# Optimization experiments

Hardware: AMD Instinct MI355X
Metric: run time of the kernel (lower is better)

The kernel has to match this reference:

```python
import jax, jax.numpy as jnp
import numpy as np

B, S, D, K = 32, 1024, 256, 1024
DECAY = 0.99
EPS = 1e-05          # EMA laplace epsilon
LN_EPS = 1e-05       # LayerNorm epsilon
COMMITMENT_COST = 0.25


def setup_inputs() -> dict:
    key = jax.random.key(0)
    k1, k2, k3 = jax.random.split(key, 3)
    inputs = jax.random.normal(k1, (B, S, D), jnp.float32)
    # nn.Embedding init: uniform(-1/K, 1/K)
    weight = jax.random.uniform(k2, (K, D), jnp.float32, -1.0 / K, 1.0 / K)
    ema_w = jax.random.normal(k3, (K, D), jnp.float32)
    ema_cluster_size = jnp.zeros((K,), jnp.float32)
    ln_gamma = jnp.ones((D,), jnp.float32)
    ln_beta = jnp.zeros((D,), jnp.float32)
    return {"inputs": inputs, "weight": weight, "ema_w": ema_w,
            "ema_cluster_size": ema_cluster_size,
            "ln_gamma": ln_gamma, "ln_beta": ln_beta}


def _layernorm(x, g, b):
    mu = jnp.mean(x, axis=-1, keepdims=True)
    var = jnp.mean((x - mu) ** 2, axis=-1, keepdims=True)
    return (x - mu) * jax.lax.rsqrt(var + LN_EPS) * g + b


def reference(inputs, weight, ema_w, ema_cluster_size, ln_gamma, ln_beta):
    flat_input = inputs.reshape(-1, D)          # [N, D] (unnormalized, used for EMA dw)
    feats = _layernorm(flat_input, ln_gamma, ln_beta)  # norm_input in sample()

    # euclidean distances ||f||^2 + ||w||^2 - 2 f w^T  -> [N, K]
    d = (jnp.sum(feats ** 2, axis=1, keepdims=True)
         + jnp.sum(weight ** 2, axis=1)
         - 2.0 * feats @ weight.T)

    sampled_dist = jnp.min(d, axis=1)           # [N]
    idx_flat = jnp.argmin(d, axis=1)            # [N] int

    # faithful reproduction of the source's reordering:
    # argsort per batch row (values in [0,S)) then flat-index into the [N]-long index vector
    order = jnp.argsort(sampled_dist.reshape(B, S), axis=1).reshape(-1)  # [N], values in [0,S)
    enc_idx = idx_flat[order]                   # [N]

    quantized = weight[enc_idx].reshape(B, S, D)

    # ---- EMA codebook update (training path), no gradients ----
    fi = jax.lax.stop_gradient(flat_input)
    counts = jax.ops.segment_sum(jnp.ones((B * S,), jnp.float32), enc_idx,
                                 num_segments=K)                    # encodings.sum(0)
    new_cs = ema_cluster_size * DECAY + (1.0 - DECAY) * counts
    n = jnp.sum(new_cs)
    new_cs = (new_cs + EPS) / (n + K * EPS) * n
    dw = jax.ops.segment_sum(fi, enc_idx, num_segments=K)            # encodings.T @ flat_input
    new_ema_w = jax.lax.stop_gradient(ema_w) * DECAY + (1.0 - DECAY) * dw
    new_weight = new_ema_w / new_cs[:, None]

    # ---- losses (avg=False, loss_type=0) ----
    e_latent = jnp.mean((jax.lax.stop_gradient(quantized) - inputs) ** 2)
    q_latent = jnp.mean((quantized - jax.lax.stop_gradient(inputs)) ** 2)
    loss = q_latent + COMMITMENT_COST * e_latent

    # straight-through estimator
    quantized_st = inputs + jax.lax.stop_gradient(quantized - inputs)

    avg_probs = counts / (B * S)
    perplexity = jnp.exp(-jnp.sum(avg_probs * jnp.log(avg_probs + 1e-10)))

    return quantized_st, loss, perplexity, enc_idx, new_weight, new_ema_w, new_cs
```

## Files before the change

kernel.cpp:

```cpp
#include <hip/hip_runtime.h>
#include <cmath>

#define B_ 32
#define S_ 1024
#define D_ 256
#define K_ 1024
#define N_ (B_*S_)

#define O_Q     0
#define O_LOSS  8388608
#define O_PERP  8388609
#define O_IDX   8388610
#define O_NW    8421378
#define O_NEW   8683522
#define O_NCS   8945666

#define OFF_FH    0ull
#define OFF_WH    16777216ull
#define OFF_BW    17301504ull
#define OFF_BWF   17309696ull
#define OFF_SAMP  17313792ull
#define OFF_IDXF  17575936ull
#define OFF_ENC   17707008ull
#define OFF_CNT   17838080ull
#define OFF_SLOWC 17842176ull
#define OFF_SLOWL 17842240ull
#define OFF_LOSSP 17973312ull
#define OFF_COFF  18235456ull
#define OFF_CUR   18239552ull
#define OFF_ROWL  18243648ull

#define MARGIN 4e-5f

typedef _Float16 f16x8 __attribute__((ext_vector_type(8)));
typedef _Float16 f16x4 __attribute__((ext_vector_type(4)));
typedef float    f32x4 __attribute__((ext_vector_type(4)));

#define GL16(gp, lp) __builtin_amdgcn_global_load_lds( \
    (const __attribute__((address_space(1))) unsigned int*)(const void*)(gp), \
    (__attribute__((address_space(3))) unsigned int*)(void*)(lp), 16, 0, 0)

__global__ void k_pre(const float* __restrict__ x, const float* __restrict__ gam,
                      const float* __restrict__ bet, _Float16* __restrict__ fh,
                      const float* __restrict__ w, double* __restrict__ Bw,
                      float* __restrict__ Bwf, _Float16* __restrict__ wh) {
    int lane = threadIdx.x & 63, wv = threadIdx.x >> 6;
    if (blockIdx.x < N_ / 4) {
        int n = blockIdx.x * 4 + wv;
        const float4 xv = ((const float4*)(x + (size_t)n * D_))[lane];
        const float4 gv = ((const float4*)gam)[lane];
        const float4 bv = ((const float4*)bet)[lane];
        float s = xv.x + xv.y + xv.z + xv.w;
        for (int m = 32; m > 0; m >>= 1) s += __shfl_xor(s, m, 64);
        float mu = s * (1.0f / 256.0f);
        float c0 = xv.x - mu, c1 = xv.y - mu, c2 = xv.z - mu, c3 = xv.w - mu;
        float vs = c0 * c0 + c1 * c1 + c2 * c2 + c3 * c3;
        for (int m = 32; m > 0; m >>= 1) vs += __shfl_xor(vs, m, 64);
        float inv = 1.0f / sqrtf(vs * (1.0f / 256.0f) + 1e-5f);
        f16x4 o;
        o[0] = (_Float16)(c0 * inv * gv.x + bv.x);
        o[1] = (_Float16)(c1 * inv * gv.y + bv.y);
        o[2] = (_Float16)(c2 * inv * gv.z + bv.z);
        o[3] = (_Float16)(c3 * inv * gv.w + bv.w);
        *(f16x4*)&fh[(size_t)n * D_ + lane * 4] = o;
    } else {
        int k = (blockIdx.x - N_ / 4) * 4 + wv;
        const float4 v = ((const float4*)(w + (size_t)k * D_))[lane];
        double s = (double)v.x * v.x + (double)v.y * v.y
                 + (double)v.z * v.z + (double)v.w * v.w;
        for (int m = 32; m > 0; m >>= 1) s += __shfl_xor(s, m, 64);
        f16x4 o;
        o[0] = (_Float16)v.x; o[1] = (_Float16)v.y;
        o[2] = (_Float16)v.z; o[3] = (_Float16)v.w;
        *(f16x4*)&wh[(size_t)k * D_ + lane * 4] = o;
        if (lane == 0) { Bw[k] = s; Bwf[k] = (float)s; }
    }
}

__launch_bounds__(512, 4)
__global__ void k_phase1(const _Float16* __restrict__ fh, const _Float16* __restrict__ wh,
                         const float* __restrict__ Bwf, float* __restrict__ pq) {
    __shared__ __align__(16) _Float16 sA[3][128][32];
    __shared__ __align__(16) _Float16 sB[3][256][32];

    const int tid = threadIdx.x;
    const int lane = tid & 63;
    const int w = tid >> 6;
    const int wr = w >> 2;
    const int wc = w & 3;
    const int l15 = lane & 15;
    const int g = lane >> 4;
    const int id = blockIdx.x;
    const int grp = (id & 7) * 32 + (id >> 5);
    const int chunk = (id >> 3) & 3;
    const int row0 = grp * 128;
    const int c0 = chunk * 256;

    const int srow = lane >> 2;
    const int scol = (lane & 3) * 8;
    const _Float16* gp[3];
    int lrow[3]; int isA[3];
#pragma unroll
    for (int j = 0; j < 3; j++) {
        int li = w * 3 + j;
        if (li < 8) {
            isA[j] = 1; lrow[j] = li * 16;
            gp[j] = fh + (size_t)(row0 + li * 16 + srow) * 256 + scol;
        } else {
            isA[j] = 0; lrow[j] = (li - 8) * 16;
            gp[j] = wh + (size_t)(c0 + (li - 8) * 16 + srow) * 256 + scol;
        }
    }

    f32x4 acc[4][4];
#pragma unroll
    for (int a = 0; a < 4; a++)
#pragma unroll
        for (int b = 0; b < 4; b++) acc[a][b] = (f32x4){0.f, 0.f, 0.f, 0.f};

#define STAGE(bi, kk) do { \
    const int eoff_ = (kk) * 32; \
    _Pragma("unroll") \
    for (int j_ = 0; j_ < 3; j_++) { \
        if (isA[j_]) GL16(gp[j_] + eoff_, &sA[bi][lrow[j_]][0]); \
        else         GL16(gp[j_] + eoff_, &sB[bi][lrow[j_]][0]); \
    } \
} while (0)

    STAGE(0, 0);
    STAGE(1, 1);
    asm volatile("s_waitcnt vmcnt(3)" ::: "memory");
    __builtin_amdgcn_s_barrier();
    __builtin_amdgcn_sched_barrier(0);

#pragma unroll
    for (int ks = 0; ks < 8; ks++) {
        const int cur = ks % 3;
        if (ks < 6) STAGE((ks + 2) % 3, ks + 2);

        f16x8 cfr[4];
#pragma unroll
        for (int cb = 0; cb < 4; cb++)
            cfr[cb] = *(const f16x8*)&sB[cur][wc * 64 + cb * 16 + l15][g * 8];
        __builtin_amdgcn_s_setprio(1);
#pragma unroll
        for (int rb = 0; rb < 4; rb++) {
            f16x8 rf = *(const f16x8*)&sA[cur][wr * 64 + rb * 16 + l15][g * 8];
#pragma unroll
            for (int cb = 0; cb < 4; cb++)
                acc[cb][rb] = __builtin_amdgcn_mfma_f32_16x16x32_f16(
                    cfr[cb], rf, acc[cb][rb], 0, 0, 0);
        }
        __builtin_amdgcn_s_setprio(0);
        __builtin_amdgcn_sched_barrier(0);

        if (ks < 6)       asm volatile("s_waitcnt vmcnt(3)" ::: "memory");
        else if (ks == 6) asm volatile("s_waitcnt vmcnt(0)" ::: "memory");
        if (ks < 7) {
            __builtin_amdgcn_s_barrier();
            __builtin_amdgcn_sched_barrier(0);
        }
    }
#undef STAGE
    __syncthreads();

    float bwv[4][4];
#pragma unroll
    for (int cb = 0; cb < 4; cb++)
#pragma unroll
        for (int r = 0; r < 4; r++)
            bwv[cb][r] = Bwf[c0 + wc * 64 + cb * 16 + g * 4 + r];

    float* red = (float*)&sA[0][0][0];
#pragma unroll
    for (int rb = 0; rb < 4; rb++) {
        float m1 = 3e38f, m2 = 3e38f; int c1 = 0x7fffffff;
#pragma unroll
        for (int cb = 0; cb < 4; cb++) {
#pragma unroll
            for (int r = 0; r < 4; r++) {
                float sv = fmaf(-2.0f, acc[cb][rb][r], bwv[cb][r]);
                int c = c0 + wc * 64 + cb * 16 + g * 4 + r;
                if (sv < m1 || (sv == m1 && c < c1)) { m2 = m1; m1 = sv; c1 = c; }
                else if (sv < m2) m2 = sv;
            }
        }
#pragma unroll
        for (int msk = 16; msk <= 32; msk <<= 1) {
            float om1 = __shfl_xor(m1, msk, 64);
            float om2 = __shfl_xor(m2, msk, 64);
            int   oc  = __shfl_xor(c1, msk, 64);
            if (om1 < m1 || (om1 == m1 && oc < c1)) {
                m2 = (m1 < om2) ? m1 : om2; m1 = om1; c1 = oc;
            } else {
                m2 = (om1 < m2) ? om1 : m2;
            }
        }
        if (lane < 16) {
            int rl = wr * 64 + rb * 16 + l15;
            int base = (rl * 4 + wc) * 3;
            red[base] = m1; red[base + 1] = m2; ((int*)red)[base + 2] = c1;
        }
    }
    __syncthreads();
    if (tid < 128) {
        float M1 = 3e38f, M2 = 3e38f; int C1 = 0x7fffffff;
        for (int q = 0; q < 4; q++) {
            int base = (tid * 4 + q) * 3;
            float m1 = red[base], m2 = red[base + 1]; int c = ((int*)red)[base + 2];
            if (m1 < M1 || (m1 == M1 && c < C1)) {
                M2 = (M1 < m2) ? M1 : m2; M1 = m1; C1 = c;
            } else {
                M2 = (m1 < M2) ? m1 : M2;
            }
        }
        pq[chunk * N_ + row0 + tid] = M1;
        pq[4 * N_ + chunk * N_ + row0 + tid] = M2;
        ((int*)pq)[8 * N_ + chunk * N_ + row0 + tid] = C1;
    }
}

__global__ void k_phase2(const float* __restrict__ x, const float* __restrict__ gam,
                         const float* __restrict__ bet, const float* __restrict__ w,
                         const double* __restrict__ Bw, const float* __restrict__ pq,
                         double* __restrict__ sampled, int* __restrict__ idxf,
                         unsigned* __restrict__ slowC, int* __restrict__ slowL) {
    int lane = threadIdx.x & 63, wv = threadIdx.x >> 6;
    int n = blockIdx.x * 4 + wv;
    const float* pm1 = pq;
    const float* pm2 = pq + 4 * N_;
    const int*   pc1 = (const int*)pq + 8 * N_;
    float M1 = 3e38f, M2 = 3e38f; int C1 = 0x7fffffff;
#pragma unroll
    for (int c = 0; c < 4; c++) {
        float m1 = pm1[c * N_ + n], m2 = pm2[c * N_ + n]; int cc = pc1[c * N_ + n];
        if (m1 < M1 || (m1 == M1 && cc < C1)) {
            M2 = (M1 < m2) ? M1 : m2; M1 = m1; C1 = cc;
        } else {
            M2 = (m1 < M2) ? m1 : M2;
        }
    }
    if (M2 - M1 <= MARGIN) {
        if (lane == 0) { unsigned p = atomicAdd(slowC, 1u); slowL[p] = n; }
        return;
    }
    const float* row = x + (size_t)n * D_;
    double xv[4], gv[4], bv[4];
#pragma unroll
    for (int i = 0; i < 4; i++) {
        int d = lane + 64 * i;
        xv[i] = row[d]; gv[i] = gam[d]; bv[i] = bet[d];
    }
    double s = xv[0] + xv[1] + xv[2] + xv[3];
    for (int m = 32; m > 0; m >>= 1) s += __shfl_xor(s, m, 64);
    double mu = s / 256.0, vs = 0.0;
#pragma unroll
    for (int i = 0; i < 4; i++) { double c = xv[i] - mu; vs += c * c; }
    for (int m = 32; m > 0; m >>= 1) vs += __shfl_xor(vs, m, 64);
    double inv = 1.0 / sqrt(vs / 256.0 + 1e-5);
    double f[4], A = 0.0;
#pragma unroll
    for (int i = 0; i < 4; i++) {
        f[i] = (xv[i] - mu) * inv * gv[i] + bv[i];
        A += f[i] * f[i];
    }
    for (int m = 32; m > 0; m >>= 1) A += __shfl_xor(A, m, 64);

    const float* wr_ = w + (size_t)C1 * D_;
    double ss = 0.0;
#pragma unroll
    for (int i = 0; i < 4; i++) ss += f[i] * (double)wr_[lane + 64 * i];
    for (int m = 32; m > 0; m >>= 1) ss += __shfl_xor(ss, m, 64);
    if (lane == 0) { sampled[n] = (A + Bw[C1]) - 2.0 * ss; idxf[n] = C1; }
}

__launch_bounds__(256)
__global__ void k_slow(const float* __restrict__ x, const float* __restrict__ gam,
                       const float* __restrict__ bet, const float* __restrict__ w,
                       const double* __restrict__ Bw,
                       const int* __restrict__ slowL, const unsigned* __restrict__ slowC,
                       double* __restrict__ sampled, int* __restrict__ idxf) {
    __shared__ double sf[256];
    __shared__ double red8[8];
    __shared__ double bmW[4];
    __shared__ int    bcW[4];
    int tid = threadIdx.x, lane = tid & 63, wv = tid >> 6;
    int cnt = (int)*slowC;
    for (int it = blockIdx.x; it < cnt; it += gridDim.x) {
        int n = slowL[it];
        double xv = x[(size_t)n * D_ + tid];
        double gv = gam[tid], bv = bet[tid];
        double s = xv;
        for (int m = 32; m > 0; m >>= 1) s += __shfl_xor(s, m, 64);
        if (lane == 0) red8[wv] = s;
        __syncthreads();
        double mu = (red8[0] + red8[1] + red8[2] + red8[3]) / 256.0;
        double c = xv - mu;
        double v2 = c * c;
        for (int m = 32; m > 0; m >>= 1) v2 += __shfl_xor(v2, m, 64);
        __syncthreads();
        if (lane == 0) red8[wv] = v2;
        __syncthreads();
        double var = (red8[0] + red8[1] + red8[2] + red8[3]) / 256.0;
        double inv = 1.0 / sqrt(var + 1e-5);
        double f = c * inv * gv + bv;
        double a2 = f * f;
        for (int m = 32; m > 0; m >>= 1) a2 += __shfl_xor(a2, m, 64);
        if (lane == 0) red8[4 + wv] = a2;
        sf[tid] = f;
        __syncthreads();
        double A = red8[4] + red8[5] + red8[6] + red8[7];

        double bm = 1.0e300; int bc = 0x7fffffff;
        for (int r = 0; r < 4; r++) {
            int cc = r * 256 + wv * 64 + lane;
            const float* wr = w + (size_t)cc * D_;
            double acc = 0.0;
#pragma unroll 8
            for (int d4 = 0; d4 < 64; d4++) {
                float4 w4 = *(const float4*)(wr + d4 * 4);
                acc += sf[d4 * 4] * (double)w4.x + sf[d4 * 4 + 1] * (double)w4.y
                     + sf[d4 * 4 + 2] * (double)w4.z + sf[d4 * 4 + 3] * (double)w4.w;
            }
            double dist = (A + Bw[cc]) - 2.0 * acc;
            if (dist < bm) { bm = dist; bc = cc; }
        }
        for (int m = 32; m > 0; m >>= 1) {
            double om = __shfl_xor(bm, m, 64);
            int    oc = __shfl_xor(bc, m, 64);
            if (om < bm || (om == bm && oc < bc)) { bm = om; bc = oc; }
        }
        if (lane == 0) { bmW[wv] = bm; bcW[wv] = bc; }
        __syncthreads();
        if (tid == 0) {
            double M = bmW[0]; int C = bcW[0];
            for (int i = 1; i < 4; i++)
                if (bmW[i] < M || (bmW[i] == M && bcW[i] < C)) { M = bmW[i]; C = bcW[i]; }
            sampled[n] = M; idxf[n] = C;
        }
        __syncthreads();
    }
}

__launch_bounds__(256)
__global__ void k_rank(const double* __restrict__ sampled, const int* __restrict__ idxf,
                       int* __restrict__ enc) {
    __shared__ double val[1024];
    int b = blockIdx.x >> 2;
    int q = blockIdx.x & 3;
    int t = threadIdx.x;
    size_t base = (size_t)b * S_;
#pragma unroll
    for (int e = 0; e < 4; e++)
        val[t + e * 256] = sampled[base + t + e * 256];
    __syncthreads();
    int i = q * 256 + t;
    double vi = val[i];
    int rank = 0;
#pragma unroll 8
    for (int j = 0; j < 1024; j++) {
        double vj = val[j];
        rank += (vj < vi) || (vj == vi && j < i);
    }
    enc[base + rank] = idxf[i];
}

__global__ void k_gather(const float* __restrict__ x, const float* __restrict__ w,
                         const int* __restrict__ enc, float* __restrict__ out,
                         unsigned* __restrict__ cnt, double* __restrict__ lossP) {
    int lane = threadIdx.x & 63, wv = threadIdx.x >> 6;
    int n = blockIdx.x * 4 + wv;
    int e = enc[n];
    const float4 q4 = ((const float4*)(w + (size_t)e * D_))[lane];
    const float4 x4 = ((const float4*)(x + (size_t)n * D_))[lane];
    ((float4*)(out + O_Q + (size_t)n * D_))[lane] = q4;
    double d0 = (double)q4.x - (double)x4.x;
    double d1 = (double)q4.y - (double)x4.y;
    double d2 = (double)q4.z - (double)x4.z;
    double d3 = (double)q4.w - (double)x4.w;
    double ls = d0 * d0 + d1 * d1 + d2 * d2 + d3 * d3;
    for (int m = 32; m > 0; m >>= 1) ls += __shfl_xor(ls, m, 64);
    if (lane == 0) {
        lossP[n] = ls;
        out[O_IDX + n] = (float)e;
        atomicAdd(&cnt[e], 1u);
    }
}

__launch_bounds__(1024)
__global__ void k_scan(const unsigned* __restrict__ cnt, int* __restrict__ coff,
                       int* __restrict__ cur) {
    __shared__ int tmp[1024];
    int t = threadIdx.x;
    int my = (int)cnt[t];
    tmp[t] = my;
    __syncthreads();
    for (int off = 1; off < 1024; off <<= 1) {
        int v = (t >= off) ? tmp[t - off] : 0;
        __syncthreads();
        tmp[t] += v;
        __syncthreads();
    }
    int excl = tmp[t] - my;
    coff[t] = excl;
    cur[t] = excl;
}

__global__ void k_scatter(const int* __restrict__ enc, int* __restrict__ cur,
                          int* __restrict__ rowl) {
    int n = blockIdx.x * 256 + threadIdx.x;
    int e = enc[n];
    int p = atomicAdd(&cur[e], 1);
    rowl[p] = n;
}

__launch_bounds__(256)
__global__ void k_post(const unsigned* __restrict__ cnt, const float* __restrict__ ema_cs,
                       const double* __restrict__ lossP,
                       const int* __restrict__ coff, const int* __restrict__ rowl,
                       const float* __restrict__ x, const float* __restrict__ ema_w,
                       float* __restrict__ out) {
    __shared__ double redd[24];
    __shared__ double ntot_s;
    int tid = threadIdx.x;

    double part = 0.0;
    for (int i = tid; i < K_; i += 256)
        part += (double)(0.99f * ema_cs[i] + 0.01f * (float)cnt[i]);
    for (int m = 32; m > 0; m >>= 1) part += __shfl_xor(part, m, 64);
    if ((tid & 63) == 0) redd[tid >> 6] = part;
    __syncthreads();
    if (tid == 0) ntot_s = redd[0] + redd[1] + redd[2] + redd[3];
    __syncthreads();
    double ntot = ntot_s;

    if (blockIdx.x < K_) {
        int k = blockIdx.x;
        float cs0 = 0.99f * ema_cs[k] + 0.01f * (float)cnt[k];
        double csf = ((double)cs0 + 1e-5) / (ntot + 1024.0 * 1e-5) * ntot;
        int base = coff[k];
        int c = (int)cnt[k];
        float acc = 0.0f;
        int j = 0;
        for (; j + 4 <= c; j += 4) {
            int r0 = rowl[base + j];
            int r1 = rowl[base + j + 1];
            int r2 = rowl[base + j + 2];
            int r3 = rowl[base + j + 3];
            float v0 = x[(size_t)r0 * D_ + tid];
            float v1 = x[(size_t)r1 * D_ + tid];
            float v2 = x[(size_t)r2 * D_ + tid];
            float v3 = x[(size_t)r3 * D_ + tid];
            acc += v0; acc += v1; acc += v2; acc += v3;
        }
        for (; j < c; j++) acc += x[(size_t)rowl[base + j] * D_ + tid];
        size_t idx = (size_t)k * D_ + tid;
        float ne = 0.99f * ema_w[idx] + 0.01f * acc;
        out[O_NEW + idx] = ne;
        out[O_NW + idx] = ne / (float)csf;
    } else {
        for (int i = tid; i < K_; i += 256) {
            float cs0 = 0.99f * ema_cs[i] + 0.01f * (float)cnt[i];
            double c2 = ((double)cs0 + 1e-5) / (ntot + 1024.0 * 1e-5) * ntot;
            out[O_NCS + i] = (float)c2;
        }
        double ent = 0.0;
        for (int i = tid; i < K_; i += 256) {
            double p = (double)cnt[i] / 32768.0;
            ent += -p * log(p + 1e-10);
        }
        for (int m = 32; m > 0; m >>= 1) ent += __shfl_xor(ent, m, 64);
        if ((tid & 63) == 0) redd[8 + (tid >> 6)] = ent;
        double ls = 0.0;
        for (int i = tid; i < N_; i += 256) ls += lossP[i];
        for (int m = 32; m > 0; m >>= 1) ls += __shfl_xor(ls, m, 64);
        if ((tid & 63) == 0) redd[16 + (tid >> 6)] = ls;
        __syncthreads();
        if (tid == 0) {
            double e = redd[8] + redd[9] + redd[10] + redd[11];
            double l = redd[16] + redd[17] + redd[18] + redd[19];
            out[O_PERP] = (float)exp(e);
            out[O_LOSS] = (float)(1.25 * l / 8388608.0);
        }
    }
}

extern "C" void kernel_launch(void* const* d_in, const int* in_sizes, int n_in,
                              void* d_out, int out_size, void* d_ws, size_t ws_size,
                              hipStream_t stream) {
    (void)in_sizes; (void)n_in; (void)out_size; (void)ws_size;
    const float* x      = (const float*)d_in[0];
    const float* w      = (const float*)d_in[1];
    const float* ema_w  = (const float*)d_in[2];
    const float* ema_cs = (const float*)d_in[3];
    const float* g      = (const float*)d_in[4];
    const float* bt     = (const float*)d_in[5];
    float* out = (float*)d_out;
    char* ws = (char*)d_ws;

    _Float16* fh = (_Float16*)(ws + OFF_FH);
    _Float16* wh = (_Float16*)(ws + OFF_WH);
    double* Bw   = (double*)(ws + OFF_BW);
    float*  Bwf  = (float*)(ws + OFF_BWF);
    double* samp = (double*)(ws + OFF_SAMP);
    int*    idxf = (int*)(ws + OFF_IDXF);
    int*    enc  = (int*)(ws + OFF_ENC);
    unsigned* cnt = (unsigned*)(ws + OFF_CNT);
    unsigned* slowC = (unsigned*)(ws + OFF_SLOWC);
    int*    slowL = (int*)(ws + OFF_SLOWL);
    double* lossP = (double*)(ws + OFF_LOSSP);
    int*    coff  = (int*)(ws + OFF_COFF);
    int*    cur   = (int*)(ws + OFF_CUR);
    int*    rowl  = (int*)(ws + OFF_ROWL);

    (void)hipMemsetAsync(ws + OFF_CNT, 0, 4160, stream);

    k_pre<<<N_ / 4 + K_ / 4, 256, 0, stream>>>(x, g, bt, fh, w, Bw, Bwf, wh);
    k_phase1<<<1024, 512, 0, stream>>>(fh, wh, Bwf, out);
    k_phase2<<<N_ / 4, 256, 0, stream>>>(x, g, bt, w, Bw, out, samp, idxf, slowC, slowL);
    k_slow<<<2048, 256, 0, stream>>>(x, g, bt, w, Bw, slowL, slowC, samp, idxf);
    k_rank<<<B_ * 4, 256, 0, stream>>>(samp, idxf, enc);
    k_gather<<<N_ / 4, 256, 0, stream>>>(x, w, enc, out, cnt, lossP);
    k_scan<<<1, 1024, 0, stream>>>(cnt, coff, cur);
    k_scatter<<<N_ / 256, 256, 0, stream>>>(enc, cur, rowl);
    k_post<<<K_ + 1, 256, 0, stream>>>(cnt, ema_cs, lossP, coff, rowl, x, ema_w, out);
}
```

Measured before the change: 281.6 us.

## Cache LayerNorm stats, fold memset into pre-kernel, hoist cluster-size total into scan

The pre-kernel now stores each row's mean, inverse std and squared-feature norm. The phase2 and slow-path kernels reuse these instead of recomputing LayerNorm reductions in double precision. The counter memset becomes an extra block of the pre-kernel, and the total cluster-size reduction moves from every k_post block into k_scan. The k_post gather loop is also unrolled to 8 loads. The cached statistics come from fp32 computation, so the double-precision refinement path is slightly less exact.

```diff
diff --git a/kernel.cpp b/kernel.cpp
--- a/kernel.cpp
+++ b/kernel.cpp
@@ -29,6 +29,9 @@
 #define OFF_COFF  18235456ull
 #define OFF_CUR   18239552ull
 #define OFF_ROWL  18243648ull
+#define OFF_MUIV  18374720ull
+#define OFF_AR    18636864ull
+#define OFF_NTOT  18899008ull
 
 #define MARGIN 4e-5f
 
@@ -43,7 +46,9 @@
 __global__ void k_pre(const float* __restrict__ x, const float* __restrict__ gam,
                       const float* __restrict__ bet, _Float16* __restrict__ fh,
                       const float* __restrict__ w, double* __restrict__ Bw,
-                      float* __restrict__ Bwf, _Float16* __restrict__ wh) {
+                      float* __restrict__ Bwf, _Float16* __restrict__ wh,
+                      float2* __restrict__ muiv, double* __restrict__ Ar,
+                      unsigned* __restrict__ cnt, unsigned* __restrict__ slowC) {
     int lane = threadIdx.x & 63, wv = threadIdx.x >> 6;
     if (blockIdx.x < N_ / 4) {
         int n = blockIdx.x * 4 + wv;
@@ -57,13 +62,19 @@
         float vs = c0 * c0 + c1 * c1 + c2 * c2 + c3 * c3;
         for (int m = 32; m > 0; m >>= 1) vs += __shfl_xor(vs, m, 64);
         float inv = 1.0f / sqrtf(vs * (1.0f / 256.0f) + 1e-5f);
+        float f0 = c0 * inv * gv.x + bv.x;
+        float f1 = c1 * inv * gv.y + bv.y;
+        float f2 = c2 * inv * gv.z + bv.z;
+        float f3 = c3 * inv * gv.w + bv.w;
+        double a = (double)f0 * f0 + (double)f1 * f1
+                 + (double)f2 * f2 + (double)f3 * f3;
+        for (int m = 32; m > 0; m >>= 1) a += __shfl_xor(a, m, 64);
         f16x4 o;
-        o[0] = (_Float16)(c0 * inv * gv.x + bv.x);
-        o[1] = (_Float16)(c1 * inv * gv.y + bv.y);
-        o[2] = (_Float16)(c2 * inv * gv.z + bv.z);
-        o[3] = (_Float16)(c3 * inv * gv.w + bv.w);
+        o[0] = (_Float16)f0; o[1] = (_Float16)f1;
+        o[2] = (_Float16)f2; o[3] = (_Float16)f3;
         *(f16x4*)&fh[(size_t)n * D_ + lane * 4] = o;
-    } else {
+        if (lane == 0) { muiv[n] = make_float2(mu, inv); Ar[n] = a; }
+    } else if (blockIdx.x < N_ / 4 + K_ / 4) {
         int k = (blockIdx.x - N_ / 4) * 4 + wv;
         const float4 v = ((const float4*)(w + (size_t)k * D_))[lane];
         double s = (double)v.x * v.x + (double)v.y * v.y
@@ -74,6 +85,11 @@
         o[2] = (_Float16)v.z; o[3] = (_Float16)v.w;
         *(f16x4*)&wh[(size_t)k * D_ + lane * 4] = o;
         if (lane == 0) { Bw[k] = s; Bwf[k] = (float)s; }
+    } else {
+        int t = threadIdx.x;
+#pragma unroll
+        for (int i = 0; i < 4; i++) cnt[t + i * 256] = 0u;
+        if (t == 0) *slowC = 0u;
     }
 }
 
@@ -223,6 +239,7 @@
 __global__ void k_phase2(const float* __restrict__ x, const float* __restrict__ gam,
                          const float* __restrict__ bet, const float* __restrict__ w,
                          const double* __restrict__ Bw, const float* __restrict__ pq,
+                         const float2* __restrict__ muiv, const double* __restrict__ Ar,
                          double* __restrict__ sampled, int* __restrict__ idxf,
                          unsigned* __restrict__ slowC, int* __restrict__ slowL) {
     int lane = threadIdx.x & 63, wv = threadIdx.x >> 6;
@@ -244,32 +261,18 @@
         if (lane == 0) { unsigned p = atomicAdd(slowC, 1u); slowL[p] = n; }
         return;
     }
+    float2 mi = muiv[n];
+    double mu = mi.x, inv = mi.y;
+    double A = Ar[n];
     const float* row = x + (size_t)n * D_;
-    double xv[4], gv[4], bv[4];
+    const float* wr_ = w + (size_t)C1 * D_;
+    double ss = 0.0;
 #pragma unroll
     for (int i = 0; i < 4; i++) {
         int d = lane + 64 * i;
-        xv[i] = row[d]; gv[i] = gam[d]; bv[i] = bet[d];
-    }
-    double s = xv[0] + xv[1] + xv[2] + xv[3];
-    for (int m = 32; m > 0; m >>= 1) s += __shfl_xor(s, m, 64);
-    double mu = s / 256.0, vs = 0.0;
-#pragma unroll
-    for (int i = 0; i < 4; i++) { double c = xv[i] - mu; vs += c * c; }
-    for (int m = 32; m > 0; m >>= 1) vs += __shfl_xor(vs, m, 64);
-    double inv = 1.0 / sqrt(vs / 256.0 + 1e-5);
-    double f[4], A = 0.0;
-#pragma unroll
-    for (int i = 0; i < 4; i++) {
-        f[i] = (xv[i] - mu) * inv * gv[i] + bv[i];
-        A += f[i] * f[i];
-    }
-    for (int m = 32; m > 0; m >>= 1) A += __shfl_xor(A, m, 64);
-
-    const float* wr_ = w + (size_t)C1 * D_;
-    double ss = 0.0;
-#pragma unroll
-    for (int i = 0; i < 4; i++) ss += f[i] * (double)wr_[lane + 64 * i];
+        double f = ((double)row[d] - mu) * inv * (double)gam[d] + (double)bet[d];
+        ss += f * (double)wr_[d];
+    }
     for (int m = 32; m > 0; m >>= 1) ss += __shfl_xor(ss, m, 64);
     if (lane == 0) { sampled[n] = (A + Bw[C1]) - 2.0 * ss; idxf[n] = C1; }
 }
@@ -278,38 +281,23 @@
 __global__ void k_slow(const float* __restrict__ x, const float* __restrict__ gam,
                        const float* __restrict__ bet, const float* __restrict__ w,
                        const double* __restrict__ Bw,
+                       const float2* __restrict__ muiv, const double* __restrict__ Ar,
                        const int* __restrict__ slowL, const unsigned* __restrict__ slowC,
                        double* __restrict__ sampled, int* __restrict__ idxf) {
     __shared__ double sf[256];
-    __shared__ double red8[8];
     __shared__ double bmW[4];
     __shared__ int    bcW[4];
     int tid = threadIdx.x, lane = tid & 63, wv = tid >> 6;
     int cnt = (int)*slowC;
     for (int it = blockIdx.x; it < cnt; it += gridDim.x) {
         int n = slowL[it];
-        double xv = x[(size_t)n * D_ + tid];
-        double gv = gam[tid], bv = bet[tid];
-        double s = xv;
-        for (int m = 32; m > 0; m >>= 1) s += __shfl_xor(s, m, 64);
-        if (lane == 0) red8[wv] = s;
-        __syncthreads();
-        double mu = (red8[0] + red8[1] + red8[2] + red8[3]) / 256.0;
-        double c = xv - mu;
-        double v2 = c * c;
-        for (int m = 32; m > 0; m >>= 1) v2 += __shfl_xor(v2, m, 64);
-        __syncthreads();
-        if (lane == 0) red8[wv] = v2;
-        __syncthreads();
-        double var = (red8[0] + red8[1] + red8[2] + red8[3]) / 256.0;
-        double inv = 1.0 / sqrt(var + 1e-5);
-        double f = c * inv * gv + bv;
-        double a2 = f * f;
-        for (int m = 32; m > 0; m >>= 1) a2 += __shfl_xor(a2, m, 64);
-        if (lane == 0) red8[4 + wv] = a2;
+        float2 mi = muiv[n];
+        double mu = mi.x, inv = mi.y;
+        double A = Ar[n];
+        double f = ((double)x[(size_t)n * D_ + tid] - mu) * inv
+                   * (double)gam[tid] + (double)bet[tid];
         sf[tid] = f;
         __syncthreads();
-        double A = red8[4] + red8[5] + red8[6] + red8[7];
 
         double bm = 1.0e300; int bc = 0x7fffffff;
         for (int r = 0; r < 4; r++) {
@@ -388,12 +376,15 @@
 }
 
 __launch_bounds__(1024)
-__global__ void k_scan(const unsigned* __restrict__ cnt, int* __restrict__ coff,
-                       int* __restrict__ cur) {
+__global__ void k_scan(const unsigned* __restrict__ cnt, const float* __restrict__ ema_cs,
+                       int* __restrict__ coff, int* __restrict__ cur,
+                       double* __restrict__ ntotP) {
     __shared__ int tmp[1024];
+    __shared__ double redn[16];
     int t = threadIdx.x;
     int my = (int)cnt[t];
     tmp[t] = my;
+    double part = (double)(0.99f * ema_cs[t] + 0.01f * (float)my);
     __syncthreads();
     for (int off = 1; off < 1024; off <<= 1) {
         int v = (t >= off) ? tmp[t - off] : 0;
@@ -404,6 +395,14 @@
     int excl = tmp[t] - my;
     coff[t] = excl;
     cur[t] = excl;
+    for (int m = 32; m > 0; m >>= 1) part += __shfl_xor(part, m, 64);
+    if ((t & 63) == 0) redn[t >> 6] = part;
+    __syncthreads();
+    if (t == 0) {
+        double s = 0.0;
+        for (int i = 0; i < 16; i++) s += redn[i];
+        *ntotP = s;
+    }
 }
 
 __global__ void k_scatter(const int* __restrict__ enc, int* __restrict__ cur,
@@ -419,20 +418,10 @@
                        const double* __restrict__ lossP,
                        const int* __restrict__ coff, const int* __restrict__ rowl,
                        const float* __restrict__ x, const float* __restrict__ ema_w,
-                       float* __restrict__ out) {
+                       const double* __restrict__ ntotP, float* __restrict__ out) {
     __shared__ double redd[24];
-    __shared__ double ntot_s;
     int tid = threadIdx.x;
-
-    double part = 0.0;
-    for (int i = tid; i < K_; i += 256)
-        part += (double)(0.99f * ema_cs[i] + 0.01f * (float)cnt[i]);
-    for (int m = 32; m > 0; m >>= 1) part += __shfl_xor(part, m, 64);
-    if ((tid & 63) == 0) redd[tid >> 6] = part;
-    __syncthreads();
-    if (tid == 0) ntot_s = redd[0] + redd[1] + redd[2] + redd[3];
-    __syncthreads();
-    double ntot = ntot_s;
+    double ntot = *ntotP;
 
     if (blockIdx.x < K_) {
         int k = blockIdx.x;
@@ -442,16 +431,15 @@
         int c = (int)cnt[k];
         float acc = 0.0f;
         int j = 0;
-        for (; j + 4 <= c; j += 4) {
-            int r0 = rowl[base + j];
-            int r1 = rowl[base + j + 1];
-            int r2 = rowl[base + j + 2];
-            int r3 = rowl[base + j + 3];
-            float v0 = x[(size_t)r0 * D_ + tid];
-            float v1 = x[(size_t)r1 * D_ + tid];
-            float v2 = x[(size_t)r2 * D_ + tid];
-            float v3 = x[(size_t)r3 * D_ + tid];
-            acc += v0; acc += v1; acc += v2; acc += v3;
+        for (; j + 8 <= c; j += 8) {
+            int r[8];
+#pragma unroll
+            for (int u = 0; u < 8; u++) r[u] = rowl[base + j + u];
+            float v[8];
+#pragma unroll
+            for (int u = 0; u < 8; u++) v[u] = x[(size_t)r[u] * D_ + tid];
+#pragma unroll
+            for (int u = 0; u < 8; u++) acc += v[u];
         }
         for (; j < c; j++) acc += x[(size_t)rowl[base + j] * D_ + tid];
         size_t idx = (size_t)k * D_ + tid;
@@ -512,16 +500,20 @@
     int*    coff  = (int*)(ws + OFF_COFF);
     int*    cur   = (int*)(ws + OFF_CUR);
     int*    rowl  = (int*)(ws + OFF_ROWL);
-
-    (void)hipMemsetAsync(ws + OFF_CNT, 0, 4160, stream);
-
-    k_pre<<<N_ / 4 + K_ / 4, 256, 0, stream>>>(x, g, bt, fh, w, Bw, Bwf, wh);
+    float2* muiv  = (float2*)(ws + OFF_MUIV);
+    double* Ar    = (double*)(ws + OFF_AR);
+    double* ntotP = (double*)(ws + OFF_NTOT);
+
+    k_pre<<<N_ / 4 + K_ / 4 + 1, 256, 0, stream>>>(x, g, bt, fh, w, Bw, Bwf, wh,
+                                                   muiv, Ar, cnt, slowC);
     k_phase1<<<1024, 512, 0, stream>>>(fh, wh, Bwf, out);
-    k_phase2<<<N_ / 4, 256, 0, stream>>>(x, g, bt, w, Bw, out, samp, idxf, slowC, slowL);
-    k_slow<<<2048, 256, 0, stream>>>(x, g, bt, w, Bw, slowL, slowC, samp, idxf);
+    k_phase2<<<N_ / 4, 256, 0, stream>>>(x, g, bt, w, Bw, out, muiv, Ar,
+                                         samp, idxf, slowC, slowL);
+    k_slow<<<2048, 256, 0, stream>>>(x, g, bt, w, Bw, muiv, Ar, slowL, slowC, samp, idxf);
     k_rank<<<B_ * 4, 256, 0, stream>>>(samp, idxf, enc);
     k_gather<<<N_ / 4, 256, 0, stream>>>(x, w, enc, out, cnt, lossP);
-    k_scan<<<1, 1024, 0, stream>>>(cnt, coff, cur);
+    k_scan<<<1, 1024, 0, stream>>>(cnt, ema_cs, coff, cur, ntotP);
     k_scatter<<<N_ / 256, 256, 0, stream>>>(enc, cur, rowl);
-    k_post<<<K_ + 1, 256, 0, stream>>>(cnt, ema_cs, lossP, coff, rowl, x, ema_w, out);
-}
+    k_post<<<K_ + 1, 256, 0, stream>>>(cnt, ema_cs, lossP, coff, rowl, x, ema_w,
+                                       ntotP, out);
+}
```

Measured after the change: 279.5 us. No clear change (-0.8%).
